# Kernel optimization log

Hardware: AMD Instinct MI355X
Metric: run time of the kernel (lower is better)

Reference implementation:

```python
import jax, jax.numpy as jnp
import numpy as np

B, S, D_IN, D_OUT, H = 4, 2048, 1024, 1024, 16
HD = D_OUT // H


def setup_inputs() -> dict:
    key = jax.random.key(0)
    ks = jax.random.split(key, 6)
    s_in = 1.0 / np.sqrt(D_IN)
    s_out = 1.0 / np.sqrt(D_OUT)
    return {
        "x": jax.random.normal(ks[0], (B, S, D_IN), dtype=jnp.float32),
        "Wq": jax.random.uniform(ks[1], (D_IN, D_OUT), jnp.float32, -s_in, s_in),
        "Wk": jax.random.uniform(ks[2], (D_IN, D_OUT), jnp.float32, -s_in, s_in),
        "Wv": jax.random.uniform(ks[3], (D_IN, D_OUT), jnp.float32, -s_in, s_in),
        "Wo": jax.random.uniform(ks[4], (D_OUT, D_OUT), jnp.float32, -s_out, s_out),
        "bo": jax.random.uniform(ks[5], (D_OUT,), jnp.float32, -s_out, s_out),
    }


def reference(x, Wq, Wk, Wv, Wo, bo):
    b, s, _ = x.shape
    # project and split heads: (b, h, s, hd)
    def heads(w):
        return (x @ w).reshape(b, s, H, HD).transpose(0, 2, 1, 3)
    q, k, v = heads(Wq), heads(Wk), heads(Wv)
    scores = jnp.einsum("bhqd,bhkd->bhqk", q, k) / np.sqrt(HD).astype(np.float32)
    causal = jnp.tril(jnp.ones((s, s), dtype=bool))  # True = keep
    scores = jnp.where(causal, scores, -jnp.inf)
    attn = jax.nn.softmax(scores, axis=-1)
    ctx = jnp.einsum("bhqk,bhkd->bhqd", attn, v)
    ctx = ctx.transpose(0, 2, 1, 3).reshape(b, s, D_OUT)
    return ctx @ Wo.T + bo
```

## Files before the change

### kernel.cpp

```cpp
#include <hip/hip_runtime.h>
#include <hip/hip_bf16.h>

#define BB   4
#define SS   2048
#define DIN  1024
#define DOUT 1024
#define NH   16
#define HDIM 64

typedef __hip_bfloat16 bf16;
typedef __attribute__((ext_vector_type(8))) short short8;
typedef __attribute__((ext_vector_type(4))) float floatx4;

#define AS1(p) ((const __attribute__((address_space(1))) void*)(p))
#define AS3(p) ((__attribute__((address_space(3))) void*)(p))

__global__ void prep_all_kernel(const float* __restrict__ x,
                                const float* __restrict__ Wq, const float* __restrict__ Wk,
                                const float* __restrict__ Wv, const float* __restrict__ Wo,
                                bf16* __restrict__ xb, bf16* __restrict__ wt,
                                bf16* __restrict__ wob) {
    __shared__ float tile[64][65];
    const int bid = blockIdx.x;
    const int tid = threadIdx.x;
    if (bid < 4096 || bid >= 4864) {
        const float* src = (bid < 4096) ? x : Wo;
        bf16* dst        = (bid < 4096) ? xb : wob;
        const int  rb    = (bid < 4096) ? bid : (bid - 4864);
        size_t i = ((size_t)rb * 256 + tid) * 8;
        float4 a = *(const float4*)(src + i);
        float4 b = *(const float4*)(src + i + 4);
        bf16 o[8] __attribute__((aligned(16)));
        o[0] = __float2bfloat16(a.x); o[1] = __float2bfloat16(a.y);
        o[2] = __float2bfloat16(a.z); o[3] = __float2bfloat16(a.w);
        o[4] = __float2bfloat16(b.x); o[5] = __float2bfloat16(b.y);
        o[6] = __float2bfloat16(b.z); o[7] = __float2bfloat16(b.w);
        *(short8*)(dst + i) = *(short8*)o;
        return;
    }
    const int pb = bid - 4096;
    const int kt = pb & 15;
    const int nt = pb >> 4;
    const int k0 = kt * 64, n0 = nt * 64;
    const float* W = (n0 < 1024) ? Wq : (n0 < 2048 ? Wk : Wv);
    const int col0 = n0 & 1023;
    {
        const int kl = tid >> 2, nc = (tid & 3) * 16;
        const float* src = W + (size_t)(k0 + kl) * 1024 + col0 + nc;
        #pragma unroll
        for (int i = 0; i < 16; i += 4) {
            float4 v = *(const float4*)(src + i);
            tile[kl][nc + i + 0] = v.x; tile[kl][nc + i + 1] = v.y;
            tile[kl][nc + i + 2] = v.z; tile[kl][nc + i + 3] = v.w;
        }
    }
    __syncthreads();
    {
        const int nl = tid >> 2, kc = (tid & 3) * 16;
        bf16 o[16] __attribute__((aligned(16)));
        #pragma unroll
        for (int i = 0; i < 16; ++i) o[i] = __float2bfloat16(tile[kc + i][nl]);
        bf16* dst = wt + (size_t)(n0 + nl) * 1024 + k0 + kc;
        *(short8*)dst       = *(short8*)&o[0];
        *(short8*)(dst + 8) = *(short8*)&o[8];
    }
}

template<int EPI>
__global__ __launch_bounds__(256) void gemm_bt_kernel(
    const bf16* __restrict__ A, const bf16* __restrict__ Bt,
    void* __restrict__ C, const float* __restrict__ bias, int K, int ldc,
    bf16* __restrict__ vt) {
    __shared__ __align__(16) bf16 As[128][64];
    __shared__ __align__(16) bf16 Bs[128][64];
    const int tid  = threadIdx.x;
    const int wave = tid >> 6, lane = tid & 63;
    const int lm   = lane & 15, quad = lane >> 4;
    const int wm   = (wave >> 1) * 64, wn = (wave & 1) * 64;
    const size_t rowA0 = (size_t)blockIdx.x * 128;
    const size_t rowB0 = (size_t)blockIdx.y * 128;

    const int srow8  = lane >> 3;
    const int schunk = (lane & 7) ^ srow8;
    const int sw     = lm & 7;

    floatx4 acc[4][4] = {};

    for (int k0 = 0; k0 < K; k0 += 64) {
        __syncthreads();
        #pragma unroll
        for (int j = 0; j < 4; ++j) {
            const int rbase = (wave * 4 + j) * 8;
            const bf16* gA = A  + (rowA0 + rbase + srow8) * (size_t)K + k0 + schunk * 8;
            __builtin_amdgcn_global_load_lds(AS1(gA), AS3(&As[rbase][0]), 16, 0, 0);
            const bf16* gB = Bt + (rowB0 + rbase + srow8) * (size_t)K + k0 + schunk * 8;
            __builtin_amdgcn_global_load_lds(AS1(gB), AS3(&Bs[rbase][0]), 16, 0, 0);
        }
        __syncthreads();
        short8 a[4][2], b[4][2];
        #pragma unroll
        for (int i = 0; i < 4; ++i) {
            const int r = wm + i * 16 + lm;
            a[i][0] = *(const short8*)&As[r][((quad    ) ^ sw) * 8];
            a[i][1] = *(const short8*)&As[r][((quad + 4) ^ sw) * 8];
        }
        #pragma unroll
        for (int j = 0; j < 4; ++j) {
            const int r = wn + j * 16 + lm;
            b[j][0] = *(const short8*)&Bs[r][((quad    ) ^ sw) * 8];
            b[j][1] = *(const short8*)&Bs[r][((quad + 4) ^ sw) * 8];
        }
        #pragma unroll
        for (int i = 0; i < 4; ++i)
            #pragma unroll
            for (int j = 0; j < 4; ++j) {
                acc[i][j] = __builtin_amdgcn_mfma_f32_16x16x32_bf16(a[i][0], b[j][0], acc[i][j], 0, 0, 0);
                acc[i][j] = __builtin_amdgcn_mfma_f32_16x16x32_bf16(a[i][1], b[j][1], acc[i][j], 0, 0, 0);
            }
    }

    if (EPI == 0 && rowB0 >= 2048) {
        #pragma unroll
        for (int i = 0; i < 4; ++i) {
            size_t row = rowA0 + wm + i * 16 + quad * 4;
            const size_t b = row >> 11;
            const int    s = (int)(row & 2047);
            #pragma unroll
            for (int j = 0; j < 4; ++j) {
                const int col = (int)(rowB0 - 2048) + wn + j * 16 + lm;
                bf16 o[4] __attribute__((aligned(8)));
                #pragma unroll
                for (int r = 0; r < 4; ++r) o[r] = __float2bfloat16(acc[i][j][r]);
                *(uint64_t*)(vt + ((b * 16 + (col >> 6)) * 64 + (col & 63)) * (size_t)SS + s)
                    = *(uint64_t*)o;
            }
        }
        return;
    }

    #pragma unroll
    for (int i = 0; i < 4; ++i) {
        size_t row = rowA0 + wm + i * 16 + quad * 4;
        #pragma unroll
        for (int j = 0; j < 4; ++j) {
            size_t col = rowB0 + wn + j * 16 + lm;
            float bv = (EPI == 1) ? bias[col] : 0.0f;
            #pragma unroll
            for (int r = 0; r < 4; ++r) {
                if (EPI == 0)
                    ((bf16*)C)[(row + r) * ldc + col] = __float2bfloat16(acc[i][j][r]);
                else
                    ((float*)C)[(row + r) * ldc + col] = acc[i][j][r] + bv;
            }
        }
    }
}

#define PSTR 68
__global__ __launch_bounds__(256, 3) void flash_attn_kernel(
    const bf16* __restrict__ qkv, const bf16* __restrict__ vt, bf16* __restrict__ ctx) {
    __shared__ __align__(16) bf16 Ks[2][64 * 64];
    __shared__ __align__(16) bf16 Vs[2][64 * 64];
    __shared__ __align__(16) bf16 Pl[4][32 * PSTR + 8];
    const int tid  = threadIdx.x;
    const int wave = tid >> 6, lane = tid & 63;
    const int lm   = lane & 15, quad = lane >> 4;

    const int id  = blockIdx.x;
    const int jl  = (id >> 3) & 7;
    const int bh  = (id & 7) * 8 + jl;
    const int p   = 15 - (id >> 6);
    const int b = bh >> 4, h = bh & 15;

    const int lane8r = lane >> 3;
    const int schunk = (lane & 7) ^ lane8r;

    const bf16* kg = qkv + (size_t)b * SS * 3072 + 1024 + h * 64 + schunk * 8;
    const bf16* vg = vt + (size_t)(b * NH + h) * 64 * SS + schunk * 8;

    bf16* Pw = &Pl[wave][0];

    const int qb = p * 128 + wave * 32;
    const int nkt = 2 * p + 2;

    short8 bq[2][2];
    #pragma unroll
    for (int g = 0; g < 2; ++g) {
        const bf16* qp = qkv + ((size_t)(b * SS + qb + g * 16 + lm)) * 3072 + h * 64 + quad * 8;
        bq[g][0] = *(const short8*)qp;
        bq[g][1] = *(const short8*)(qp + 32);
    }

    floatx4 o[2][4] = {};
    float lsum[2] = {0.f, 0.f};

    #pragma unroll
    for (int c = 0; c < 2; ++c) {
        const int row = c * 32 + wave * 8 + lane8r;
        __builtin_amdgcn_global_load_lds(AS1(kg + (size_t)row * 3072), AS3(&Ks[0][(c * 256 + wave * 64) * 8]), 16, 0, 0);
        __builtin_amdgcn_global_load_lds(AS1(vg + (size_t)row * SS), AS3(&Vs[0][(c * 256 + wave * 64) * 8]), 16, 0, 0);
    }

    #pragma unroll 1
    for (int kt = 0; kt < nkt; ++kt) {
        const int cur = kt & 1;
        __syncthreads();
        if (kt + 1 < nkt) {
            #pragma unroll
            for (int c = 0; c < 2; ++c) {
                const int row = c * 32 + wave * 8 + lane8r;
                __builtin_amdgcn_global_load_lds(AS1(kg + (size_t)((kt + 1) * 64 + row) * 3072),
                                                 AS3(&Ks[cur ^ 1][(c * 256 + wave * 64) * 8]), 16, 0, 0);
                __builtin_amdgcn_global_load_lds(AS1(vg + (size_t)row * SS + (kt + 1) * 64),
                                                 AS3(&Vs[cur ^ 1][(c * 256 + wave * 64) * 8]), 16, 0, 0);
            }
        }

        const int sw = lm & 7;
        const bf16* Ksb = &Ks[cur][0];
        const bf16* Vsb = &Vs[cur][0];
        short8 ka[4][2], va[4][2];
        #pragma unroll
        for (int nt = 0; nt < 4; ++nt) {
            const int r0 = (nt * 16 + lm) * 64;
            ka[nt][0] = *(const short8*)(Ksb + r0 + ((quad ^ sw) * 8));
            ka[nt][1] = *(const short8*)(Ksb + r0 + (((4 + quad) ^ sw) * 8));
            va[nt][0] = *(const short8*)(Vsb + r0 + ((quad ^ sw) * 8));
            va[nt][1] = *(const short8*)(Vsb + r0 + (((4 + quad) ^ sw) * 8));
        }

        #pragma unroll
        for (int g = 0; g < 2; ++g) {
            floatx4 sc[4];
            #pragma unroll
            for (int nt = 0; nt < 4; ++nt) {
                floatx4 z = {};
                z = __builtin_amdgcn_mfma_f32_16x16x32_bf16(ka[nt][0], bq[g][0], z, 0, 0, 0);
                z = __builtin_amdgcn_mfma_f32_16x16x32_bf16(ka[nt][1], bq[g][1], z, 0, 0, 0);
                sc[nt] = z;
            }
            if (kt * 64 + 63 > qb + g * 16) {
                const int qrow = qb + g * 16 + lm;
                #pragma unroll
                for (int nt = 0; nt < 4; ++nt)
                    #pragma unroll
                    for (int r = 0; r < 4; ++r)
                        if (kt * 64 + nt * 16 + quad * 4 + r > qrow) sc[nt][r] = -1e30f;
            }
            #pragma unroll
            for (int nt = 0; nt < 4; ++nt) {
                bf16 pk[4] __attribute__((aligned(8)));
                #pragma unroll
                for (int r = 0; r < 4; ++r) {
                    float pv = __builtin_amdgcn_exp2f(sc[nt][r] * 0.18033688f);
                    lsum[g] += pv;
                    pk[r] = __float2bfloat16(pv);
                }
                *(uint64_t*)&Pw[(g * 16 + lm) * PSTR + nt * 16 + quad * 4] = *(uint64_t*)pk;
            }
        }
        #pragma unroll
        for (int g = 0; g < 2; ++g) {
            const short8 ap0 = *(const short8*)&Pw[(g * 16 + lm) * PSTR + quad * 8];
            const short8 ap1 = *(const short8*)&Pw[(g * 16 + lm) * PSTR + 32 + quad * 8];
            #pragma unroll
            for (int t = 0; t < 4; ++t) {
                o[g][t] = __builtin_amdgcn_mfma_f32_16x16x32_bf16(ap0, va[t][0], o[g][t], 0, 0, 0);
                o[g][t] = __builtin_amdgcn_mfma_f32_16x16x32_bf16(ap1, va[t][1], o[g][t], 0, 0, 0);
            }
        }
    }

    #pragma unroll
    for (int g = 0; g < 2; ++g) {
        float rsum = lsum[g];
        rsum += __shfl_xor(rsum, 16);
        rsum += __shfl_xor(rsum, 32);
        float rl[4];
        #pragma unroll
        for (int r = 0; r < 4; ++r) rl[r] = 1.0f / __shfl(rsum, quad * 4 + r);
        #pragma unroll
        for (int t = 0; t < 4; ++t)
            #pragma unroll
            for (int r = 0; r < 4; ++r) {
                size_t row = (size_t)b * SS + qb + g * 16 + quad * 4 + r;
                ctx[row * 1024 + h * 64 + t * 16 + lm] = __float2bfloat16(o[g][t][r] * rl[r]);
            }
    }
}

extern "C" void kernel_launch(void* const* d_in, const int* in_sizes, int n_in,
                              void* d_out, int out_size, void* d_ws, size_t ws_size,
                              hipStream_t stream) {
    const float* x  = (const float*)d_in[0];
    const float* Wq = (const float*)d_in[1];
    const float* Wk = (const float*)d_in[2];
    const float* Wv = (const float*)d_in[3];
    const float* Wo = (const float*)d_in[4];
    const float* bo = (const float*)d_in[5];

    char* ws = (char*)d_ws;
    bf16* xb  = (bf16*)ws;  ws += (size_t)8192 * 1024 * 2;
    bf16* wt  = (bf16*)ws;  ws += (size_t)3072 * 1024 * 2;
    bf16* wob = (bf16*)ws;  ws += (size_t)1024 * 1024 * 2;
    bf16* qkv = (bf16*)ws;  ws += (size_t)8192 * 3072 * 2;
    bf16* vtb = (bf16*)ws;  ws += (size_t)BB * NH * HDIM * SS * 2;
    bf16* ctx = xb;

    prep_all_kernel<<<5376, 256, 0, stream>>>(x, Wq, Wk, Wv, Wo, xb, wt, wob);
    gemm_bt_kernel<0><<<dim3(64, 24), 256, 0, stream>>>(xb, wt, (void*)qkv, nullptr, 1024, 3072, vtb);
    flash_attn_kernel<<<1024, 256, 0, stream>>>(qkv, vtb, ctx);
    gemm_bt_kernel<1><<<dim3(64, 8), 256, 0, stream>>>(ctx, wob, d_out, bo, 1024, 1024, nullptr);
}
```

Before: 252.0 us.

## Double-buffer GEMM LDS tiles, skip masked attention tiles per wave, raise MFMA priority

The projection GEMM now uses two LDS buffers so the global-to-LDS load of the next K tile overlaps the MFMAs on the current one, which removes one barrier per iteration. In the attention kernel, a wave skips the compute for key tiles lying entirely above its causal diagonal. s_setprio calls bracket the MFMA blocks so waves doing matrix math get scheduling priority. The cost is twice the GEMM LDS footprint, which may lower occupancy.

```diff
diff --git a/kernel.cpp b/kernel.cpp
--- a/kernel.cpp
+++ b/kernel.cpp
@@ -71,8 +71,8 @@
     const bf16* __restrict__ A, const bf16* __restrict__ Bt,
     void* __restrict__ C, const float* __restrict__ bias, int K, int ldc,
     bf16* __restrict__ vt) {
-    __shared__ __align__(16) bf16 As[128][64];
-    __shared__ __align__(16) bf16 Bs[128][64];
+    __shared__ __align__(16) bf16 As[2][128][64];
+    __shared__ __align__(16) bf16 Bs[2][128][64];
     const int tid  = threadIdx.x;
     const int wave = tid >> 6, lane = tid & 63;
     const int lm   = lane & 15, quad = lane >> 4;
@@ -86,30 +86,44 @@
 
     floatx4 acc[4][4] = {};
 
-    for (int k0 = 0; k0 < K; k0 += 64) {
+    #pragma unroll
+    for (int j = 0; j < 4; ++j) {
+        const int rbase = (wave * 4 + j) * 8;
+        const bf16* gA = A  + (rowA0 + rbase + srow8) * (size_t)K + schunk * 8;
+        __builtin_amdgcn_global_load_lds(AS1(gA), AS3(&As[0][rbase][0]), 16, 0, 0);
+        const bf16* gB = Bt + (rowB0 + rbase + srow8) * (size_t)K + schunk * 8;
+        __builtin_amdgcn_global_load_lds(AS1(gB), AS3(&Bs[0][rbase][0]), 16, 0, 0);
+    }
+
+    const int nk = K >> 6;
+    #pragma unroll 1
+    for (int t = 0; t < nk; ++t) {
+        const int cur = t & 1;
         __syncthreads();
-        #pragma unroll
-        for (int j = 0; j < 4; ++j) {
-            const int rbase = (wave * 4 + j) * 8;
-            const bf16* gA = A  + (rowA0 + rbase + srow8) * (size_t)K + k0 + schunk * 8;
-            __builtin_amdgcn_global_load_lds(AS1(gA), AS3(&As[rbase][0]), 16, 0, 0);
-            const bf16* gB = Bt + (rowB0 + rbase + srow8) * (size_t)K + k0 + schunk * 8;
-            __builtin_amdgcn_global_load_lds(AS1(gB), AS3(&Bs[rbase][0]), 16, 0, 0);
-        }
-        __syncthreads();
+        if (t + 1 < nk) {
+            #pragma unroll
+            for (int j = 0; j < 4; ++j) {
+                const int rbase = (wave * 4 + j) * 8;
+                const bf16* gA = A  + (rowA0 + rbase + srow8) * (size_t)K + (t + 1) * 64 + schunk * 8;
+                __builtin_amdgcn_global_load_lds(AS1(gA), AS3(&As[cur ^ 1][rbase][0]), 16, 0, 0);
+                const bf16* gB = Bt + (rowB0 + rbase + srow8) * (size_t)K + (t + 1) * 64 + schunk * 8;
+                __builtin_amdgcn_global_load_lds(AS1(gB), AS3(&Bs[cur ^ 1][rbase][0]), 16, 0, 0);
+            }
+        }
         short8 a[4][2], b[4][2];
         #pragma unroll
         for (int i = 0; i < 4; ++i) {
             const int r = wm + i * 16 + lm;
-            a[i][0] = *(const short8*)&As[r][((quad    ) ^ sw) * 8];
-            a[i][1] = *(const short8*)&As[r][((quad + 4) ^ sw) * 8];
+            a[i][0] = *(const short8*)&As[cur][r][((quad    ) ^ sw) * 8];
+            a[i][1] = *(const short8*)&As[cur][r][((quad + 4) ^ sw) * 8];
         }
         #pragma unroll
         for (int j = 0; j < 4; ++j) {
             const int r = wn + j * 16 + lm;
-            b[j][0] = *(const short8*)&Bs[r][((quad    ) ^ sw) * 8];
-            b[j][1] = *(const short8*)&Bs[r][((quad + 4) ^ sw) * 8];
-        }
+            b[j][0] = *(const short8*)&Bs[cur][r][((quad    ) ^ sw) * 8];
+            b[j][1] = *(const short8*)&Bs[cur][r][((quad + 4) ^ sw) * 8];
+        }
+        __builtin_amdgcn_s_setprio(1);
         #pragma unroll
         for (int i = 0; i < 4; ++i)
             #pragma unroll
@@ -117,6 +131,7 @@
                 acc[i][j] = __builtin_amdgcn_mfma_f32_16x16x32_bf16(a[i][0], b[j][0], acc[i][j], 0, 0, 0);
                 acc[i][j] = __builtin_amdgcn_mfma_f32_16x16x32_bf16(a[i][1], b[j][1], acc[i][j], 0, 0, 0);
             }
+        __builtin_amdgcn_s_setprio(0);
     }
 
     if (EPI == 0 && rowB0 >= 2048) {
@@ -216,6 +231,8 @@
             }
         }
 
+        if (kt * 64 > qb + 31) continue;
+
         const int sw = lm & 7;
         const bf16* Ksb = &Ks[cur][0];
         const bf16* Vsb = &Vs[cur][0];
@@ -232,6 +249,7 @@
         #pragma unroll
         for (int g = 0; g < 2; ++g) {
             floatx4 sc[4];
+            __builtin_amdgcn_s_setprio(1);
             #pragma unroll
             for (int nt = 0; nt < 4; ++nt) {
                 floatx4 z = {};
@@ -239,6 +257,7 @@
                 z = __builtin_amdgcn_mfma_f32_16x16x32_bf16(ka[nt][1], bq[g][1], z, 0, 0, 0);
                 sc[nt] = z;
             }
+            __builtin_amdgcn_s_setprio(0);
             if (kt * 64 + 63 > qb + g * 16) {
                 const int qrow = qb + g * 16 + lm;
                 #pragma unroll
@@ -263,11 +282,13 @@
         for (int g = 0; g < 2; ++g) {
             const short8 ap0 = *(const short8*)&Pw[(g * 16 + lm) * PSTR + quad * 8];
             const short8 ap1 = *(const short8*)&Pw[(g * 16 + lm) * PSTR + 32 + quad * 8];
+            __builtin_amdgcn_s_setprio(1);
             #pragma unroll
             for (int t = 0; t < 4; ++t) {
                 o[g][t] = __builtin_amdgcn_mfma_f32_16x16x32_bf16(ap0, va[t][0], o[g][t], 0, 0, 0);
                 o[g][t] = __builtin_amdgcn_mfma_f32_16x16x32_bf16(ap1, va[t][1], o[g][t], 0, 0, 0);
             }
+            __builtin_amdgcn_s_setprio(0);
         }
     }
 
```

Result: no change. 249.8 us (-0.9%).
